# Optimization experiments

Measured on AMD Instinct MI355X. Metric: run time of the kernel, lower is better.

## Reference

```python
import jax, jax.numpy as jnp
import numpy as np


def setup_inputs() -> dict:
    key = jax.random.key(0)
    k1, k2, k3 = jax.random.split(key, 3)
    B, D, N, C = 4096, 256, 65536, 10
    x = jax.random.normal(k1, (B, D), dtype=jnp.float32)
    keys = jax.random.normal(k2, (N, D), dtype=jnp.float32)
    values = jax.random.uniform(k3, (N, C), dtype=jnp.float32)
    return {"x": x, "keys": keys, "values": values, "k": 8}


def reference(x, keys, values, k):
    # squared euclidean distances [B, N] without materializing diff cube:
    x_sq = jnp.sum(x * x, axis=1, keepdims=True)          # [B,1]
    k_sq = jnp.sum(keys * keys, axis=1)                   # [N]
    dists = x_sq - 2.0 * (x @ keys.T) + k_sq[None, :]     # [B,N]
    neg_top, indices = jax.lax.top_k(-dists, k)           # [B,k]
    hit_values = values[indices]                          # [B,k,C]
    return jnp.sum(hit_values, axis=1) / jnp.float32(k)   # [B,C]
```

## Files before the change

### kernel.cpp

```cpp
#include <hip/hip_runtime.h>
#include <stdint.h>
#include <float.h>

#define B_ROWS 4096
#define N_KEYS 65536
#define DDIM 256
#define NCH 10

#define NSPLIT 8
#define SPLIT_KEYS (N_KEYS / NSPLIT)
#define ROWS_PER_BLK 64
#define CHUNK_KEYS 64
#define NCHUNK (SPLIT_KEYS / CHUNK_KEYS)

typedef float f32x4 __attribute__((ext_vector_type(4)));
typedef short bf16x8 __attribute__((ext_vector_type(8)));

static __device__ __forceinline__ unsigned short f2bf(float f) {
  unsigned u = __float_as_uint(f);
  return (unsigned short)((u + 0x7FFFu + ((u >> 16) & 1u)) >> 16);
}
static __device__ __forceinline__ unsigned ford(float f) {
  unsigned u = __float_as_uint(f);
  return u ^ ((unsigned)((int)u >> 31) | 0x80000000u);
}
static __device__ __forceinline__ unsigned long long shfl_xor_u64(unsigned long long v, int m) {
  unsigned lo = __shfl_xor((unsigned)v, m, 64);
  unsigned hi = __shfl_xor((unsigned)(v >> 32), m, 64);
  return ((unsigned long long)hi << 32) | lo;
}
static __device__ __forceinline__ double shfl_xor_f64(double v, int m) {
  return __longlong_as_double((long long)shfl_xor_u64((unsigned long long)__double_as_longlong(v), m));
}
static __device__ __forceinline__ void gl_lds16(const void* g, void* l) {
  __builtin_amdgcn_global_load_lds(
      (const __attribute__((address_space(1))) unsigned int*)g,
      (__attribute__((address_space(3))) unsigned int*)l, 16, 0, 0);
}

__global__ __launch_bounds__(256) void transpose_keys(const float* __restrict__ keys,
                                                      unsigned char* __restrict__ kbf,
                                                      float* __restrict__ ksq) {
  __shared__ __align__(16) unsigned char T[128 * 512];
  const int t = threadIdx.x;
  const int lane = t & 63;
  const float4* src = (const float4*)(keys + (size_t)blockIdx.x * 128 * DDIM);
#pragma unroll
  for (int j = 0; j < 32; ++j) {
    int g = j * 256 + t;
    float4 v = src[g];
    int key = g >> 6;
    int u = lane >> 1, sub = lane & 1;
    unsigned lo = ((unsigned)f2bf(v.y) << 16) | f2bf(v.x);
    unsigned hi2 = ((unsigned)f2bf(v.w) << 16) | f2bf(v.z);
    unsigned long long p = ((unsigned long long)hi2 << 32) | lo;
    *(unsigned long long*)&T[key * 512 + ((u ^ (key & 7)) << 4) + (sub << 3)] = p;
    float ss = v.x * v.x + v.y * v.y + v.z * v.z + v.w * v.w;
#pragma unroll
    for (int off = 32; off; off >>= 1) ss += __shfl_xor(ss, off, 64);
    if (lane == 0) ksq[blockIdx.x * 128 + key] = ss;
  }
  __syncthreads();
  uint4* dst = (uint4*)(kbf + (size_t)blockIdx.x * 65536);
#pragma unroll
  for (int j = 0; j < 16; ++j) {
    int ou = j * 256 + t;
    int c64 = ou >> 11, rem = ou & 2047;
    int koct = rem >> 6, key64 = rem & 63;
    int keyl = c64 * 64 + key64;
    dst[ou] = *(const uint4*)&T[keyl * 512 + ((koct ^ (keyl & 7)) << 4)];
  }
}

__global__ __launch_bounds__(512, 4) void knn_main(
    const float* __restrict__ x,
    const unsigned char* __restrict__ kbf,
    const float* __restrict__ ksqg,
    unsigned int* __restrict__ pools,
    unsigned int* __restrict__ counts,
    int CAP) {
  __shared__ __align__(16) unsigned char tiles[2][32768];
  __shared__ float tauh[2][2][16][4];
  __shared__ unsigned int rowcnt[64];

  const int t = threadIdx.x;
  const int lane = t & 63;
  const int wv = t >> 6;
  const int mw = wv & 3;
  const int ws = wv >> 2;
  const int lo4 = lane & 15;
  const int hi = lane >> 4;

  const int split = blockIdx.x & (NSPLIT - 1);
  const int rb = (blockIdx.x >> 3) * ROWS_PER_BLK;
  const int sb = split * SPLIT_KEYS;
  const int rot = ((blockIdx.x >> 8) & 1) * (NCHUNK / 2);

  const int xrow0 = rb + ws * 32 + lo4;
  const int xrow1 = xrow0 + 16;
  const int rl0 = ws * 32 + lo4, rl1 = rl0 + 16;

  bf16x8 xb0[8], xb1[8];
#pragma unroll
  for (int s = 0; s < 8; ++s) {
    const float* p0 = x + (size_t)xrow0 * DDIM + s * 32 + hi * 8;
    const float* p1 = x + (size_t)xrow1 * DDIM + s * 32 + hi * 8;
    float4 a = *(const float4*)p0, b = *(const float4*)(p0 + 4);
    float4 c = *(const float4*)p1, d = *(const float4*)(p1 + 4);
    union { unsigned short us[8]; bf16x8 v; } u0, u1;
    u0.us[0]=f2bf(-2.f*a.x); u0.us[1]=f2bf(-2.f*a.y); u0.us[2]=f2bf(-2.f*a.z); u0.us[3]=f2bf(-2.f*a.w);
    u0.us[4]=f2bf(-2.f*b.x); u0.us[5]=f2bf(-2.f*b.y); u0.us[6]=f2bf(-2.f*b.z); u0.us[7]=f2bf(-2.f*b.w);
    u1.us[0]=f2bf(-2.f*c.x); u1.us[1]=f2bf(-2.f*c.y); u1.us[2]=f2bf(-2.f*c.z); u1.us[3]=f2bf(-2.f*c.w);
    u1.us[4]=f2bf(-2.f*d.x); u1.us[5]=f2bf(-2.f*d.y); u1.us[6]=f2bf(-2.f*d.z); u1.us[7]=f2bf(-2.f*d.w);
    xb0[s] = u0.v; xb1[s] = u1.v;
  }

  if (t < 64) rowcnt[t] = 0;

  float smin0 = FLT_MAX, smin1 = FLT_MAX;
  const unsigned char* srcbase = kbf + ((size_t)(split * NCHUNK) << 15);
  const size_t pb0 = ((size_t)xrow0 * NSPLIT + split) * (size_t)CAP;
  const size_t pb1 = ((size_t)xrow1 * NSPLIT + split) * (size_t)CAP;

  auto CIDX = [&](int c) { return (c + rot) & (NCHUNK - 1); };

  auto STAGE = [&](int c, int buf) {
    const unsigned char* src = srcbase + ((size_t)CIDX(c) << 15);
    unsigned char* wb = (unsigned char*)tiles[buf] + ((wv * 64) << 4);
#pragma unroll
    for (int i = 0; i < 4; ++i)
      gl_lds16(src + (((i * 512) + t) << 4), wb + ((i * 512) << 4));
  };
  auto LOADQ = [&](int c) {
    return *(const float4*)(ksqg + sb + CIDX(c) * CHUNK_KEYS + mw * 16 + hi * 4);
  };

  f32x4 a0, a1;
  float4 kqc, kqn;

  auto COMPUTE = [&](int c) {
    const unsigned char* tile = tiles[c & 1];
    f32x4 ini;
    ini[0] = kqc.x; ini[1] = kqc.y; ini[2] = kqc.z; ini[3] = kqc.w;
    a0 = ini; a1 = ini;
    __builtin_amdgcn_s_setprio(1);
#pragma unroll
    for (int s = 0; s < 8; ++s) {
      const unsigned char* rp = tile + (s * 4 + hi) * 1024 + (mw * 16 + lo4) * 16;
      bf16x8 af = *(const bf16x8*)rp;
      a0 = __builtin_amdgcn_mfma_f32_16x16x32_bf16(af, xb0[s], a0, 0, 0, 0);
      a1 = __builtin_amdgcn_mfma_f32_16x16x32_bf16(af, xb1[s], a1, 0, 0, 0);
    }
    __builtin_amdgcn_s_setprio(0);
  };

  auto SEL = [&](int c, bool append, float tau0, float tau1) {
    float mb0 = fminf(fminf(a0[0], a0[1]), fminf(a0[2], a0[3]));
    float mb1 = fminf(fminf(a1[0], a1[1]), fminf(a1[2], a1[3]));
    smin0 = fminf(smin0, mb0);
    smin1 = fminf(smin1, mb1);
    if (append) {
      const int kloc = CIDX(c) * CHUNK_KEYS + mw * 16 + hi * 4;
      if (mb0 <= tau0) {
#pragma unroll
        for (int i = 0; i < 4; ++i) {
          if (a0[i] <= tau0) {
            unsigned slot = atomicAdd(&rowcnt[rl0], 1u);
            if ((int)slot < CAP)
              pools[pb0 + slot] = (ford(a0[i]) & 0xFFFFE000u) | (unsigned)(kloc + i);
          }
        }
      }
      if (mb1 <= tau1) {
#pragma unroll
        for (int i = 0; i < 4; ++i) {
          if (a1[i] <= tau1) {
            unsigned slot = atomicAdd(&rowcnt[rl1], 1u);
            if ((int)slot < CAP)
              pools[pb1 + slot] = (ford(a1[i]) & 0xFFFFE000u) | (unsigned)(kloc + i);
          }
        }
      }
    }
  };

  auto RDTAU = [&](float& tau0, float& tau1) {
    float4 t0 = *(const float4*)&tauh[0][ws][lo4][0];
    float4 t1 = *(const float4*)&tauh[1][ws][lo4][0];
    tau0 = fmaxf(fmaxf(t0.x, t0.y), fmaxf(t0.z, t0.w));
    tau1 = fmaxf(fmaxf(t1.x, t1.y), fmaxf(t1.z, t1.w));
  };

  auto PUBLISH = [&]() {
    float p0 = fminf(smin0, __shfl_xor(smin0, 16, 64));
    p0 = fmaxf(p0, __shfl_xor(p0, 32, 64));
    float p1 = fminf(smin1, __shfl_xor(smin1, 16, 64));
    p1 = fmaxf(p1, __shfl_xor(p1, 32, 64));
    if (hi == 0) {
      tauh[0][ws][lo4][mw] = p0;
      tauh[1][ws][lo4][mw] = p1;
    }
  };

  STAGE(0, 0);
  kqc = LOADQ(0);
  __syncthreads();
  STAGE(1, 1);
  kqn = LOADQ(1);
  COMPUTE(0);
  SEL(0, false, 0.f, 0.f);
  PUBLISH();
  __syncthreads();
  {
    float tau0, tau1;
    RDTAU(tau0, tau1);
    SEL(0, true, tau0, tau1);
  }
  kqc = kqn;

#pragma unroll 1
  for (int c = 1; c < NCHUNK; ++c) {
    const int cn = (c + 1 < NCHUNK) ? c + 1 : c;
    STAGE(cn, (c + 1) & 1);
    kqn = LOADQ(cn);
    float tau0, tau1;
    RDTAU(tau0, tau1);
    COMPUTE(c);
    SEL(c, true, tau0, tau1);
    if (c & 1) PUBLISH();
    kqc = kqn;
    __syncthreads();
  }

  __syncthreads();
  if (t < 64) counts[(size_t)(rb + t) * NSPLIT + split] = rowcnt[t];
}

__global__ __launch_bounds__(64) void knn_refine(
    const float* __restrict__ x,
    const float* __restrict__ keys,
    const float* __restrict__ ksq,
    const float* __restrict__ values,
    const unsigned int* __restrict__ pools,
    const unsigned int* __restrict__ counts,
    int CAP,
    float* __restrict__ out) {
  __shared__ float4 xl[64];
  const int row = blockIdx.x;
  const int lane = threadIdx.x;

  xl[lane] = ((const float4*)(x + (size_t)row * DDIM))[lane];
  __syncthreads();

  unsigned long long h[8];
#pragma unroll
  for (int i = 0; i < 8; ++i) h[i] = ~0ULL;

  auto insert = [&](unsigned long long v) {
    if (v < h[7]) {
#pragma unroll
      for (int j = 7; j >= 1; --j) {
        unsigned long long a = h[j - 1];
        unsigned long long mx = a > v ? a : v;
        h[j] = (v < h[j]) ? mx : h[j];
      }
      h[0] = h[0] < v ? h[0] : v;
    }
  };

  for (int s = 0; s < NSPLIT; ++s) {
    unsigned cnt = counts[(size_t)row * NSPLIT + s];
    if ((int)cnt <= CAP) {
      const unsigned int* pp = pools + ((size_t)row * NSPLIT + s) * (size_t)CAP;
      for (int i = lane; i < (int)cnt; i += 64) {
        unsigned p = pp[i];
        unsigned long long v = ((unsigned long long)p << 17)
                             | (unsigned)(s * SPLIT_KEYS + (p & 0x1FFFu));
        insert(v);
      }
    } else {
      for (int kk = lane; kk < SPLIT_KEYS; kk += 64) {
        int gk = s * SPLIT_KEYS + kk;
        const float4* kr = (const float4*)(keys + (size_t)gk * DDIM);
        float acc = 0.f;
#pragma unroll 8
        for (int d = 0; d < 64; ++d) {
          float4 kv = kr[d], xv = xl[d];
          acc = fmaf(kv.x, xv.x, acc); acc = fmaf(kv.y, xv.y, acc);
          acc = fmaf(kv.z, xv.z, acc); acc = fmaf(kv.w, xv.w, acc);
        }
        float sc = fmaf(-2.0f, acc, ksq[gk]);
        unsigned p = (ford(sc) & 0xFFFFE000u) | (unsigned)kk;
        insert(((unsigned long long)p << 17) | (unsigned)gk);
      }
    }
  }

  int myidx = 0;
#pragma unroll 1
  for (int r = 0; r < 24; ++r) {
    unsigned long long m = h[0];
#pragma unroll
    for (int off = 32; off; off >>= 1) {
      unsigned long long o = shfl_xor_u64(m, off);
      m = o < m ? o : m;
    }
    if (lane == r) myidx = (int)(m & 0x1FFFFu);
    if (h[0] == m) {
#pragma unroll
      for (int i = 0; i < 7; ++i) h[i] = h[i + 1];
      h[7] = ~0ULL;
    }
  }

  double dv = 1e300;
  if (lane < 24) {
    const float4* kr = (const float4*)(keys + (size_t)myidx * DDIM);
    double s = 0.0;
#pragma unroll 8
    for (int d = 0; d < 64; ++d) {
      float4 kv = kr[d], xv = xl[d];
      double d0 = (double)xv.x - (double)kv.x;
      double d1 = (double)xv.y - (double)kv.y;
      double d2 = (double)xv.z - (double)kv.z;
      double d3 = (double)xv.w - (double)kv.w;
      s += d0 * d0 + d1 * d1 + d2 * d2 + d3 * d3;
    }
    dv = s;
  }

  int di = myidx;
  int chosen[8];
#pragma unroll
  for (int r = 0; r < 8; ++r) {
    double m = dv; int mi = di;
#pragma unroll
    for (int off = 32; off; off >>= 1) {
      double om = shfl_xor_f64(m, off);
      int omi = __shfl_xor(mi, off, 64);
      if (om < m || (om == m && omi < mi)) { m = om; mi = omi; }
    }
    chosen[r] = mi;
    if (di == mi && dv < 1e300) dv = 1e300;
  }

  if (lane < NCH) {
    double a = 0.0;
#pragma unroll
    for (int r = 0; r < 8; ++r) a += (double)values[(size_t)chosen[r] * NCH + lane];
    out[row * NCH + lane] = (float)(a * 0.125);
  }
}

extern "C" void kernel_launch(void* const* d_in, const int* in_sizes, int n_in,
                              void* d_out, int out_size, void* d_ws, size_t ws_size,
                              hipStream_t stream) {
  (void)in_sizes; (void)n_in; (void)out_size;
  const float* x      = (const float*)d_in[0];
  const float* keys   = (const float*)d_in[1];
  const float* values = (const float*)d_in[2];
  float* out = (float*)d_out;

  char* ws = (char*)d_ws;
  unsigned char* kbf = (unsigned char*)ws;
  float* ksq   = (float*)(ws + 33554432);
  unsigned int* counts = (unsigned int*)(ws + 33554432 + 262144);
  unsigned int* pools  = (unsigned int*)(ws + 33554432 + 262144 + 131072);

  size_t base = 33554432 + 262144 + 131072;
  size_t cap = (ws_size > base) ? (ws_size - base) / ((size_t)B_ROWS * NSPLIT * 4) : 32;
  if (cap < 32) cap = 32;
  if (cap > 2048) cap = 2048;
  int CAP = (int)cap;

  transpose_keys<<<N_KEYS / 128, 256, 0, stream>>>(keys, kbf, ksq);
  knn_main<<<(B_ROWS / ROWS_PER_BLK) * NSPLIT, 512, 0, stream>>>(
      x, kbf, ksq, pools, counts, CAP);
  knn_refine<<<B_ROWS, 64, 0, stream>>>(x, keys, ksq, values, pools, counts, CAP, out);
}
```

Before: 301.3 us.

## Use 128-row blocks, 16 key splits, 32-key chunks with 4-deep staging pipeline

Reshapes the main KNN kernel so each block covers 128 query rows over a 16-way key split, processing 32-key chunks. Key staging goes from double buffering with a full barrier per chunk to a 4-buffer ring gated by vmcnt waits and a raw s_barrier, to overlap loads with MFMA compute. The threshold is now seeded from two sample chunks, the per-row pool cap changes, and the packed pool entries carry 12 bits of key index with one more bit of distance. Risks include more pool overflow or fallback work in refine, and correctness of the hand-managed waitcnt pipeline.

New measurement: 276.3 us (median of 3 runs). 1.09x faster.

```diff
diff --git a/kernel.cpp b/kernel.cpp
--- a/kernel.cpp
+++ b/kernel.cpp
@@ -7,10 +7,10 @@
 #define DDIM 256
 #define NCH 10
 
-#define NSPLIT 8
+#define NSPLIT 16
 #define SPLIT_KEYS (N_KEYS / NSPLIT)
-#define ROWS_PER_BLK 64
-#define CHUNK_KEYS 64
+#define ROWS_PER_BLK 128
+#define CHUNK_KEYS 32
 #define NCHUNK (SPLIT_KEYS / CHUNK_KEYS)
 
 typedef float f32x4 __attribute__((ext_vector_type(4)));
@@ -61,13 +61,13 @@
     if (lane == 0) ksq[blockIdx.x * 128 + key] = ss;
   }
   __syncthreads();
-  uint4* dst = (uint4*)(kbf + (size_t)blockIdx.x * 65536);
+  uint4* dst = (uint4*)kbf + (size_t)blockIdx.x * 4096;
 #pragma unroll
   for (int j = 0; j < 16; ++j) {
     int ou = j * 256 + t;
-    int c64 = ou >> 11, rem = ou & 2047;
-    int koct = rem >> 6, key64 = rem & 63;
-    int keyl = c64 * 64 + key64;
+    int rec = ou >> 10, rem = ou & 1023;
+    int koct = rem >> 5, key32 = rem & 31;
+    int keyl = rec * 32 + key32;
     dst[ou] = *(const uint4*)&T[keyl * 512 + ((koct ^ (keyl & 7)) << 4)];
   }
 }
@@ -79,22 +79,21 @@
     unsigned int* __restrict__ pools,
     unsigned int* __restrict__ counts,
     int CAP) {
-  __shared__ __align__(16) unsigned char tiles[2][32768];
-  __shared__ float tauh[2][2][16][4];
-  __shared__ unsigned int rowcnt[64];
+  __shared__ __align__(16) unsigned char tiles[4][16384];
+  __shared__ float tauh[2][4][16][2];
+  __shared__ unsigned int rowcnt[128];
 
   const int t = threadIdx.x;
   const int lane = t & 63;
   const int wv = t >> 6;
-  const int mw = wv & 3;
-  const int ws = wv >> 2;
+  const int mw = wv & 1;
+  const int ws = wv >> 1;
   const int lo4 = lane & 15;
   const int hi = lane >> 4;
 
   const int split = blockIdx.x & (NSPLIT - 1);
-  const int rb = (blockIdx.x >> 3) * ROWS_PER_BLK;
+  const int rb = (blockIdx.x >> 4) * ROWS_PER_BLK;
   const int sb = split * SPLIT_KEYS;
-  const int rot = ((blockIdx.x >> 8) & 1) * (NCHUNK / 2);
 
   const int xrow0 = rb + ws * 32 + lo4;
   const int xrow1 = xrow0 + 16;
@@ -115,38 +114,36 @@
     xb0[s] = u0.v; xb1[s] = u1.v;
   }
 
-  if (t < 64) rowcnt[t] = 0;
+  if (t < 128) rowcnt[t] = 0;
 
   float smin0 = FLT_MAX, smin1 = FLT_MAX;
-  const unsigned char* srcbase = kbf + ((size_t)(split * NCHUNK) << 15);
+  const unsigned char* srcbase = kbf + ((size_t)(split * NCHUNK) << 14);
   const size_t pb0 = ((size_t)xrow0 * NSPLIT + split) * (size_t)CAP;
   const size_t pb1 = ((size_t)xrow1 * NSPLIT + split) * (size_t)CAP;
 
-  auto CIDX = [&](int c) { return (c + rot) & (NCHUNK - 1); };
-
   auto STAGE = [&](int c, int buf) {
-    const unsigned char* src = srcbase + ((size_t)CIDX(c) << 15);
-    unsigned char* wb = (unsigned char*)tiles[buf] + ((wv * 64) << 4);
-#pragma unroll
-    for (int i = 0; i < 4; ++i)
-      gl_lds16(src + (((i * 512) + t) << 4), wb + ((i * 512) << 4));
+    const unsigned char* src = srcbase + ((size_t)c << 14);
+#pragma unroll
+    for (int i = 0; i < 2; ++i)
+      gl_lds16(src + (((i * 512) + t) << 4),
+               (unsigned char*)tiles[buf] + ((i * 512 + wv * 64) << 4));
   };
   auto LOADQ = [&](int c) {
-    return *(const float4*)(ksqg + sb + CIDX(c) * CHUNK_KEYS + mw * 16 + hi * 4);
+    return *(const float4*)(ksqg + sb + c * CHUNK_KEYS + mw * 16 + hi * 4);
   };
 
   f32x4 a0, a1;
   float4 kqc, kqn;
 
-  auto COMPUTE = [&](int c) {
-    const unsigned char* tile = tiles[c & 1];
+  auto COMPUTE = [&](int buf) {
+    const unsigned char* tile = tiles[buf];
     f32x4 ini;
     ini[0] = kqc.x; ini[1] = kqc.y; ini[2] = kqc.z; ini[3] = kqc.w;
     a0 = ini; a1 = ini;
     __builtin_amdgcn_s_setprio(1);
 #pragma unroll
     for (int s = 0; s < 8; ++s) {
-      const unsigned char* rp = tile + (s * 4 + hi) * 1024 + (mw * 16 + lo4) * 16;
+      const unsigned char* rp = tile + (s * 4 + hi) * 512 + (mw * 16 + lo4) * 16;
       bf16x8 af = *(const bf16x8*)rp;
       a0 = __builtin_amdgcn_mfma_f32_16x16x32_bf16(af, xb0[s], a0, 0, 0, 0);
       a1 = __builtin_amdgcn_mfma_f32_16x16x32_bf16(af, xb1[s], a1, 0, 0, 0);
@@ -160,14 +157,14 @@
     smin0 = fminf(smin0, mb0);
     smin1 = fminf(smin1, mb1);
     if (append) {
-      const int kloc = CIDX(c) * CHUNK_KEYS + mw * 16 + hi * 4;
+      const int kloc = c * CHUNK_KEYS + mw * 16 + hi * 4;
       if (mb0 <= tau0) {
 #pragma unroll
         for (int i = 0; i < 4; ++i) {
           if (a0[i] <= tau0) {
             unsigned slot = atomicAdd(&rowcnt[rl0], 1u);
             if ((int)slot < CAP)
-              pools[pb0 + slot] = (ford(a0[i]) & 0xFFFFE000u) | (unsigned)(kloc + i);
+              pools[pb0 + slot] = (ford(a0[i]) & 0xFFFFF000u) | (unsigned)(kloc + i);
           }
         }
       }
@@ -177,7 +174,7 @@
           if (a1[i] <= tau1) {
             unsigned slot = atomicAdd(&rowcnt[rl1], 1u);
             if ((int)slot < CAP)
-              pools[pb1 + slot] = (ford(a1[i]) & 0xFFFFE000u) | (unsigned)(kloc + i);
+              pools[pb1 + slot] = (ford(a1[i]) & 0xFFFFF000u) | (unsigned)(kloc + i);
           }
         }
       }
@@ -185,16 +182,14 @@
   };
 
   auto RDTAU = [&](float& tau0, float& tau1) {
-    float4 t0 = *(const float4*)&tauh[0][ws][lo4][0];
-    float4 t1 = *(const float4*)&tauh[1][ws][lo4][0];
-    tau0 = fmaxf(fmaxf(t0.x, t0.y), fmaxf(t0.z, t0.w));
-    tau1 = fmaxf(fmaxf(t1.x, t1.y), fmaxf(t1.z, t1.w));
+    tau0 = fmaxf(tauh[0][ws][lo4][0], tauh[0][ws][lo4][1]);
+    tau1 = fmaxf(tauh[1][ws][lo4][0], tauh[1][ws][lo4][1]);
   };
 
   auto PUBLISH = [&]() {
-    float p0 = fminf(smin0, __shfl_xor(smin0, 16, 64));
+    float p0 = fmaxf(smin0, __shfl_xor(smin0, 16, 64));
     p0 = fmaxf(p0, __shfl_xor(p0, 32, 64));
-    float p1 = fminf(smin1, __shfl_xor(smin1, 16, 64));
+    float p1 = fmaxf(smin1, __shfl_xor(smin1, 16, 64));
     p1 = fmaxf(p1, __shfl_xor(p1, 32, 64));
     if (hi == 0) {
       tauh[0][ws][lo4][mw] = p0;
@@ -203,37 +198,36 @@
   };
 
   STAGE(0, 0);
+  STAGE(64, 1);
+  __syncthreads();
   kqc = LOADQ(0);
+  COMPUTE(0); SEL(0, false, 0.f, 0.f);
+  kqc = LOADQ(64);
+  COMPUTE(1); SEL(64, false, 0.f, 0.f);
+  PUBLISH();
   __syncthreads();
   STAGE(1, 1);
+  STAGE(2, 2);
+  kqc = LOADQ(0);
   kqn = LOADQ(1);
-  COMPUTE(0);
-  SEL(0, false, 0.f, 0.f);
-  PUBLISH();
-  __syncthreads();
-  {
+
+#pragma unroll 1
+  for (int c = 0; c < NCHUNK; ++c) {
+    asm volatile("s_waitcnt vmcnt(4)" ::: "memory");
+    __builtin_amdgcn_s_barrier();
     float tau0, tau1;
     RDTAU(tau0, tau1);
-    SEL(0, true, tau0, tau1);
-  }
-  kqc = kqn;
-
-#pragma unroll 1
-  for (int c = 1; c < NCHUNK; ++c) {
-    const int cn = (c + 1 < NCHUNK) ? c + 1 : c;
-    STAGE(cn, (c + 1) & 1);
-    kqn = LOADQ(cn);
-    float tau0, tau1;
-    RDTAU(tau0, tau1);
-    COMPUTE(c);
+    COMPUTE(c & 3);
     SEL(c, true, tau0, tau1);
     if (c & 1) PUBLISH();
     kqc = kqn;
-    __syncthreads();
-  }
-
-  __syncthreads();
-  if (t < 64) counts[(size_t)(rb + t) * NSPLIT + split] = rowcnt[t];
+    kqn = LOADQ((c + 2 < NCHUNK) ? c + 2 : 0);
+    const int cs = (c + 3 < NCHUNK) ? c + 3 : c + 3 - NCHUNK;
+    STAGE(cs, (c + 3) & 3);
+  }
+
+  __syncthreads();
+  if (t < 128) counts[(size_t)(rb + t) * NSPLIT + split] = rowcnt[t];
 }
 
 __global__ __launch_bounds__(64) void knn_refine(
@@ -274,9 +268,8 @@
       const unsigned int* pp = pools + ((size_t)row * NSPLIT + s) * (size_t)CAP;
       for (int i = lane; i < (int)cnt; i += 64) {
         unsigned p = pp[i];
-        unsigned long long v = ((unsigned long long)p << 17)
-                             | (unsigned)(s * SPLIT_KEYS + (p & 0x1FFFu));
-        insert(v);
+        unsigned gk = (unsigned)(s * SPLIT_KEYS) + (p & 0xFFFu);
+        insert(((unsigned long long)(p & 0xFFFFF000u) << 16) | gk);
       }
     } else {
       for (int kk = lane; kk < SPLIT_KEYS; kk += 64) {
@@ -290,8 +283,7 @@
           acc = fmaf(kv.z, xv.z, acc); acc = fmaf(kv.w, xv.w, acc);
         }
         float sc = fmaf(-2.0f, acc, ksq[gk]);
-        unsigned p = (ford(sc) & 0xFFFFE000u) | (unsigned)kk;
-        insert(((unsigned long long)p << 17) | (unsigned)gk);
+        insert(((unsigned long long)(ford(sc) & 0xFFFFF000u) << 16) | (unsigned)gk);
       }
     }
   }
@@ -305,7 +297,7 @@
       unsigned long long o = shfl_xor_u64(m, off);
       m = o < m ? o : m;
     }
-    if (lane == r) myidx = (int)(m & 0x1FFFFu);
+    if (lane == r) myidx = (int)(m & 0xFFFFu);
     if (h[0] == m) {
 #pragma unroll
       for (int i = 0; i < 7; ++i) h[i] = h[i + 1];
@@ -365,12 +357,12 @@
   unsigned char* kbf = (unsigned char*)ws;
   float* ksq   = (float*)(ws + 33554432);
   unsigned int* counts = (unsigned int*)(ws + 33554432 + 262144);
-  unsigned int* pools  = (unsigned int*)(ws + 33554432 + 262144 + 131072);
-
-  size_t base = 33554432 + 262144 + 131072;
-  size_t cap = (ws_size > base) ? (ws_size - base) / ((size_t)B_ROWS * NSPLIT * 4) : 32;
-  if (cap < 32) cap = 32;
-  if (cap > 2048) cap = 2048;
+  unsigned int* pools  = (unsigned int*)(ws + 33554432 + 262144 + 262144);
+
+  size_t base = 33554432 + 262144 + 262144;
+  size_t cap = (ws_size > base) ? (ws_size - base) / ((size_t)B_ROWS * NSPLIT * 4) : 60;
+  if (cap < 60) cap = 60;
+  if (cap > 512) cap = 512;
   int CAP = (int)cap;
 
   transpose_keys<<<N_KEYS / 128, 256, 0, stream>>>(keys, kbf, ksq);
```
